# Performance work log

Hardware: AMD Instinct MI355X
Metric: run time of the kernel (lower is better)

Reference implementation:

```python
import jax, jax.numpy as jnp
import numpy as np

IN_FEATURES_LS = (8, 16, 32, 64, 128)
OUT_FEATURES = 512
MAX_FEAT = max(IN_FEATURES_LS)


def setup_inputs() -> dict:
    key = jax.random.key(0)
    k_x, k_idx, k_w, k_b = jax.random.split(key, 4)
    B, S = 16, 2048
    x = jax.random.normal(k_x, (B, S, MAX_FEAT), dtype=jnp.float32)
    # actual patch size per token: sample an index into in_features_ls
    idx = jax.random.randint(k_idx, (B, S), 0, len(IN_FEATURES_LS))
    in_feat_size = jnp.array(IN_FEATURES_LS, dtype=jnp.int64)[idx]
    weight = jax.random.normal(k_w, (len(IN_FEATURES_LS), OUT_FEATURES, MAX_FEAT), dtype=jnp.float32) * 0.05
    bias = jax.random.normal(k_b, (len(IN_FEATURES_LS), OUT_FEATURES), dtype=jnp.float32) * 0.05
    return {"x": x, "in_feat_size": in_feat_size, "weight": weight, "bias": bias}


def reference(x, in_feat_size, weight, bias):
    sizes = jnp.asarray(IN_FEATURES_LS)                       # [K]
    # mask padding columns of each expert's weight: [K, max_feat]
    feat_mask = (jnp.arange(MAX_FEAT)[None, :] < sizes[:, None]).astype(x.dtype)
    w = weight * feat_mask[:, None, :]                        # [K, out, max_feat]
    # all K projections computed unconditionally (faithful to original)
    y = jnp.einsum('bsi,koi->bsko', x, w) + bias              # [B, S, K, out]
    sel = (in_feat_size[..., None] == sizes).astype(x.dtype)  # [B, S, K] one-hot
    return jnp.einsum('bsko,bsk->bso', y, sel)                # [B, S, out]
```

## Files before the change

kernel.cpp:

```cpp
#include <hip/hip_runtime.h>

#define NEXP 5
#define MAXF 128
#define NOUT 512
#define TPB  64
#define PITCH 136

typedef __attribute__((ext_vector_type(8))) short short8;
typedef __attribute__((ext_vector_type(4))) float floatx4;

__device__ __forceinline__ ushort f2bf(float f) {
    uint u = __float_as_uint(f);
    u += 0x7FFF + ((u >> 16) & 1);
    return (ushort)(u >> 16);
}

__global__ __launch_bounds__(256) void misl_pack(
    const float* __restrict__ w, ushort* __restrict__ wb) {
    const int idx = blockIdx.x * 256 + threadIdx.x;
    const int lane = idx & 63, nb16 = (idx >> 6) & 31;
    const int s = (idx >> 11) & 3, e = idx >> 13;
    if (e < NEXP) {
        const int ncol = nb16 * 16 + (lane & 15);
        const int k0 = s * 32 + (lane >> 4) * 8;
        const int K = 8 << e;
        const float* wr = w + ((size_t)e * NOUT + ncol) * MAXF + k0;
        short8 v;
        #pragma unroll
        for (int j = 0; j < 8; ++j)
            v[j] = (short)((k0 + j < K) ? f2bf(wr[j]) : (ushort)0);
        *(short8*)(wb + (size_t)idx * 8) = v;
    }
}

template <int E>
__device__ __forceinline__ void run_expert(
    const ushort* __restrict__ xs, const int* __restrict__ perm,
    const ushort* __restrict__ wb, const float* __restrict__ b,
    float* __restrict__ out, int t0, int boff, int c, int lane, int n_base) {
    constexpr int NS = (E == 4) ? 4 : (E == 3) ? 2 : 1;
    const int m = lane & 15, q = lane >> 4;
    const int nb16 = n_base >> 4;
    const ushort* wbe = wb + (size_t)E * 4 * 32 * 64 * 8;

    short8 bf[NS][4];
    #pragma unroll
    for (int s = 0; s < NS; ++s)
        #pragma unroll
        for (int bi = 0; bi < 4; ++bi)
            bf[s][bi] = *(const short8*)(wbe + ((size_t)(s * 32 + nb16 + bi) * 64 + lane) * 8);
    float bv[4];
    #pragma unroll
    for (int bi = 0; bi < 4; ++bi) bv[bi] = b[E * NOUT + n_base + bi * 16 + m];

    for (int o = 0; o < c; o += 16) {
        const int L = (c - o > 16) ? 16 : (c - o);
        const int idx = (m < L) ? m : (L - 1);
        const int row = perm[boff + o + idx];
        const ushort* xr = xs + (size_t)row * PITCH + q * 8;
        floatx4 acc[4];
        #pragma unroll
        for (int bi = 0; bi < 4; ++bi)
            acc[bi] = floatx4{bv[bi], bv[bi], bv[bi], bv[bi]};
        #pragma unroll
        for (int s = 0; s < NS; ++s) {
            const short8 af = *(const short8*)(xr + s * 32);
            #pragma unroll
            for (int bi = 0; bi < 4; ++bi)
                acc[bi] = __builtin_amdgcn_mfma_f32_16x16x32_bf16(af, bf[s][bi], acc[bi], 0, 0, 0);
        }
        #pragma unroll
        for (int r = 0; r < 4; ++r) {
            const int mi = q * 4 + r;
            if (mi < L) {
                const int tr = perm[boff + o + mi];
                float* orow = out + (size_t)(t0 + tr) * NOUT + n_base + m;
                #pragma unroll
                for (int bi = 0; bi < 4; ++bi) orow[bi * 16] = acc[bi][r];
            }
        }
    }
}

__global__ __launch_bounds__(512) void misl_main(
    const float* __restrict__ x, const int* __restrict__ feat,
    const ushort* __restrict__ wb, const float* __restrict__ b,
    float* __restrict__ out, int n) {
    __shared__ ushort xs[TPB * PITCH];
    __shared__ int perm[TPB];
    __shared__ int cnt[NEXP];
    __shared__ int base[NEXP];

    const int tid = threadIdx.x;
    const int t0 = blockIdx.x * TPB;
    const int nt = (n - t0 < TPB) ? (n - t0) : TPB;

    if (tid < NEXP) cnt[tid] = 0;

    const int row = tid >> 3;
    const int colu = (tid & 7) * 16;
    float4 a0, a1, a2, a3;
    const bool stg = (row < nt);
    if (stg) {
        const float* xp = x + (size_t)(t0 + row) * MAXF + colu;
        a0 = *(const float4*)xp;
        a1 = *(const float4*)(xp + 4);
        a2 = *(const float4*)(xp + 8);
        a3 = *(const float4*)(xp + 12);
    }
    __syncthreads();

    int e = 0, r = 0;
    if (tid < nt) {
        e = __ffs((uint)feat[t0 + tid]) - 4;
        r = atomicAdd(&cnt[e], 1);
    }
    if (stg) {
        short8 v0, v1;
        v0[0] = (short)f2bf(a0.x); v0[1] = (short)f2bf(a0.y);
        v0[2] = (short)f2bf(a0.z); v0[3] = (short)f2bf(a0.w);
        v0[4] = (short)f2bf(a1.x); v0[5] = (short)f2bf(a1.y);
        v0[6] = (short)f2bf(a1.z); v0[7] = (short)f2bf(a1.w);
        v1[0] = (short)f2bf(a2.x); v1[1] = (short)f2bf(a2.y);
        v1[2] = (short)f2bf(a2.z); v1[3] = (short)f2bf(a2.w);
        v1[4] = (short)f2bf(a3.x); v1[5] = (short)f2bf(a3.y);
        v1[6] = (short)f2bf(a3.z); v1[7] = (short)f2bf(a3.w);
        *(short8*)(xs + (size_t)row * PITCH + colu)     = v0;
        *(short8*)(xs + (size_t)row * PITCH + colu + 8) = v1;
    }
    __syncthreads();
    if (tid == 0) {
        int o = 0;
        #pragma unroll
        for (int j = NEXP - 1; j >= 0; --j) { base[j] = o; o += cnt[j]; }
    }
    __syncthreads();
    if (tid < nt) perm[base[e] + r] = tid;
    __syncthreads();

    const int lane = tid & 63;
    const int n_base = (tid >> 6) * 64;
    const int c0 = cnt[0], c1 = cnt[1], c2 = cnt[2], c3 = cnt[3], c4 = cnt[4];
    const int b0 = base[0], b1 = base[1], b2 = base[2], b3 = base[3], b4 = base[4];

    if (c4) run_expert<4>(xs, perm, wb, b, out, t0, b4, c4, lane, n_base);
    if (c3) run_expert<3>(xs, perm, wb, b, out, t0, b3, c3, lane, n_base);
    if (c2) run_expert<2>(xs, perm, wb, b, out, t0, b2, c2, lane, n_base);
    if (c1) run_expert<1>(xs, perm, wb, b, out, t0, b1, c1, lane, n_base);
    if (c0) run_expert<0>(xs, perm, wb, b, out, t0, b0, c0, lane, n_base);
}

extern "C" void kernel_launch(void* const* d_in, const int* in_sizes, int n_in,
                              void* d_out, int out_size, void* d_ws, size_t ws_size,
                              hipStream_t stream) {
    const float* x    = (const float*)d_in[0];
    const int*   feat = (const int*)d_in[1];
    const float* w    = (const float*)d_in[2];
    const float* b    = (const float*)d_in[3];
    float* out = (float*)d_out;
    ushort* wb = (ushort*)d_ws;

    const int n = in_sizes[1];
    misl_pack<<<160, 256, 0, stream>>>(w, wb);
    misl_main<<<(n + TPB - 1) / TPB, 512, 0, stream>>>(x, feat, wb, b, out, n);
}
```

Measured before the change: 94.82 us.

## Swap MFMA operands for row-contiguous float4 stores and double tokens per block

Swaps the MFMA A/B operands so each lane holds four consecutive output columns of one token. Each lane can then write its results as floatx4 vector stores instead of scattered scalar stores, and the bias becomes a vector load. Tokens per block go from 64 to 128, which halves the grid and amortises the per-block register load of weight fragments over more tokens. The bigger tile doubles LDS use and cuts the number of blocks, which can reduce latency hiding.

```diff
diff --git a/kernel.cpp b/kernel.cpp
--- a/kernel.cpp
+++ b/kernel.cpp
@@ -3,7 +3,7 @@
 #define NEXP 5
 #define MAXF 128
 #define NOUT 512
-#define TPB  64
+#define TPB  128
 #define PITCH 136
 
 typedef __attribute__((ext_vector_type(8))) short short8;
@@ -43,15 +43,16 @@
     const int nb16 = n_base >> 4;
     const ushort* wbe = wb + (size_t)E * 4 * 32 * 64 * 8;
 
-    short8 bf[NS][4];
+    short8 wf[NS][4];
     #pragma unroll
     for (int s = 0; s < NS; ++s)
         #pragma unroll
         for (int bi = 0; bi < 4; ++bi)
-            bf[s][bi] = *(const short8*)(wbe + ((size_t)(s * 32 + nb16 + bi) * 64 + lane) * 8);
-    float bv[4];
+            wf[s][bi] = *(const short8*)(wbe + ((size_t)(s * 32 + nb16 + bi) * 64 + lane) * 8);
+    floatx4 bv[4];
     #pragma unroll
-    for (int bi = 0; bi < 4; ++bi) bv[bi] = b[E * NOUT + n_base + bi * 16 + m];
+    for (int bi = 0; bi < 4; ++bi)
+        bv[bi] = *(const floatx4*)(b + E * NOUT + n_base + bi * 16 + q * 4);
 
     for (int o = 0; o < c; o += 16) {
         const int L = (c - o > 16) ? 16 : (c - o);
@@ -60,24 +61,19 @@
         const ushort* xr = xs + (size_t)row * PITCH + q * 8;
         floatx4 acc[4];
         #pragma unroll
-        for (int bi = 0; bi < 4; ++bi)
-            acc[bi] = floatx4{bv[bi], bv[bi], bv[bi], bv[bi]};
+        for (int bi = 0; bi < 4; ++bi) acc[bi] = bv[bi];
         #pragma unroll
         for (int s = 0; s < NS; ++s) {
-            const short8 af = *(const short8*)(xr + s * 32);
+            const short8 xf = *(const short8*)(xr + s * 32);
             #pragma unroll
             for (int bi = 0; bi < 4; ++bi)
-                acc[bi] = __builtin_amdgcn_mfma_f32_16x16x32_bf16(af, bf[s][bi], acc[bi], 0, 0, 0);
+                acc[bi] = __builtin_amdgcn_mfma_f32_16x16x32_bf16(wf[s][bi], xf, acc[bi], 0, 0, 0);
         }
-        #pragma unroll
-        for (int r = 0; r < 4; ++r) {
-            const int mi = q * 4 + r;
-            if (mi < L) {
-                const int tr = perm[boff + o + mi];
-                float* orow = out + (size_t)(t0 + tr) * NOUT + n_base + m;
-                #pragma unroll
-                for (int bi = 0; bi < 4; ++bi) orow[bi * 16] = acc[bi][r];
-            }
+        if (m < L) {
+            float* orow = out + (size_t)(t0 + row) * NOUT + n_base + q * 4;
+            #pragma unroll
+            for (int bi = 0; bi < 4; ++bi)
+                *(floatx4*)(orow + bi * 16) = acc[bi];
         }
     }
 }
@@ -97,16 +93,28 @@
 
     if (tid < NEXP) cnt[tid] = 0;
 
-    const int row = tid >> 3;
-    const int colu = (tid & 7) * 16;
-    float4 a0, a1, a2, a3;
-    const bool stg = (row < nt);
-    if (stg) {
+    const int row = tid >> 2;
+    const int colu = (tid & 3) * 32;
+    if (row < nt) {
         const float* xp = x + (size_t)(t0 + row) * MAXF + colu;
-        a0 = *(const float4*)xp;
-        a1 = *(const float4*)(xp + 4);
-        a2 = *(const float4*)(xp + 8);
-        a3 = *(const float4*)(xp + 12);
+        #pragma unroll
+        for (int h = 0; h < 2; ++h) {
+            const float4 a0 = *(const float4*)(xp + h * 16);
+            const float4 a1 = *(const float4*)(xp + h * 16 + 4);
+            const float4 a2 = *(const float4*)(xp + h * 16 + 8);
+            const float4 a3 = *(const float4*)(xp + h * 16 + 12);
+            short8 v0, v1;
+            v0[0] = (short)f2bf(a0.x); v0[1] = (short)f2bf(a0.y);
+            v0[2] = (short)f2bf(a0.z); v0[3] = (short)f2bf(a0.w);
+            v0[4] = (short)f2bf(a1.x); v0[5] = (short)f2bf(a1.y);
+            v0[6] = (short)f2bf(a1.z); v0[7] = (short)f2bf(a1.w);
+            v1[0] = (short)f2bf(a2.x); v1[1] = (short)f2bf(a2.y);
+            v1[2] = (short)f2bf(a2.z); v1[3] = (short)f2bf(a2.w);
+            v1[4] = (short)f2bf(a3.x); v1[5] = (short)f2bf(a3.y);
+            v1[6] = (short)f2bf(a3.z); v1[7] = (short)f2bf(a3.w);
+            *(short8*)(xs + (size_t)row * PITCH + colu + h * 16)     = v0;
+            *(short8*)(xs + (size_t)row * PITCH + colu + h * 16 + 8) = v1;
+        }
     }
     __syncthreads();
 
@@ -114,19 +122,6 @@
     if (tid < nt) {
         e = __ffs((uint)feat[t0 + tid]) - 4;
         r = atomicAdd(&cnt[e], 1);
-    }
-    if (stg) {
-        short8 v0, v1;
-        v0[0] = (short)f2bf(a0.x); v0[1] = (short)f2bf(a0.y);
-        v0[2] = (short)f2bf(a0.z); v0[3] = (short)f2bf(a0.w);
-        v0[4] = (short)f2bf(a1.x); v0[5] = (short)f2bf(a1.y);
-        v0[6] = (short)f2bf(a1.z); v0[7] = (short)f2bf(a1.w);
-        v1[0] = (short)f2bf(a2.x); v1[1] = (short)f2bf(a2.y);
-        v1[2] = (short)f2bf(a2.z); v1[3] = (short)f2bf(a2.w);
-        v1[4] = (short)f2bf(a3.x); v1[5] = (short)f2bf(a3.y);
-        v1[6] = (short)f2bf(a3.z); v1[7] = (short)f2bf(a3.w);
-        *(short8*)(xs + (size_t)row * PITCH + colu)     = v0;
-        *(short8*)(xs + (size_t)row * PITCH + colu + 8) = v1;
     }
     __syncthreads();
     if (tid == 0) {
```

Result: slower. 97.20 us (+2.5%).
